# Kernel optimization log

Hardware: AMD Instinct MI355X
Metric: run time of the kernel (lower is better)

## Reference

```python
import jax, jax.numpy as jnp
import numpy as np

N_NODES = 100000
N_EDGES = 625000
D = 128


def setup_inputs() -> dict:
    key = jax.random.key(0)
    ks = jax.random.split(key, 6)
    x = jax.random.normal(ks[0], (N_NODES, D), dtype=jnp.float32)
    src = jax.random.randint(ks[1], (N_EDGES,), 0, N_NODES, dtype=jnp.int32)
    dst = jnp.sort(jax.random.randint(ks[2], (N_EDGES,), 0, N_NODES, dtype=jnp.int32))
    edge_w = jax.random.uniform(ks[3], (N_EDGES,), dtype=jnp.float32)
    # linear layer params (fan-in scaled)
    W = jax.random.normal(ks[4], (D, D), dtype=jnp.float32) / np.sqrt(D)
    b = jnp.zeros((D,), dtype=jnp.float32)
    # highway gate params (glorot-uniform-ish range as in source)
    init_range = np.sqrt(2.0 / (D + D)).astype(np.float32)
    kernel_gate = jax.random.uniform(ks[5], (D, D), dtype=jnp.float32,
                                     minval=-init_range, maxval=init_range)
    bias_gate = jnp.zeros((D,), dtype=jnp.float32)
    return {"x": x, "src": src, "dst": dst, "edge_w": edge_w,
            "W": W, "b": b, "kernel_gate": kernel_gate, "bias_gate": bias_gate}


def reference(x, src, dst, edge_w, W, b, kernel_gate, bias_gate):
    # hidden = Linear(x); dropout is identity in eval mode
    hidden = x @ W.T + b                                  # [N, D]
    # support = spmm(adj, hidden): gather src rows, weight, scatter-add to dst
    msgs = edge_w[:, None] * hidden[src]                  # [E, D]
    support = jax.ops.segment_sum(msgs, dst, num_segments=x.shape[0])
    support = jax.nn.relu(support)                        # act
    # highway gate
    gate = jax.nn.sigmoid(x @ kernel_gate + bias_gate)    # [N, D]
    out = gate * support + (1.0 - gate) * x
    return out
```

## Files before the change

kernel.cpp:

```cpp
#include <hip/hip_runtime.h>

#define DD 128

typedef __attribute__((ext_vector_type(8))) short bf16x8;
typedef __attribute__((ext_vector_type(4))) float f32x4;

__device__ __forceinline__ unsigned int cvt_pk_bf16(float lo, float hi) {
  unsigned int r;
  asm("v_cvt_pk_bf16_f32 %0, %1, %2" : "=v"(r) : "v"(lo), "v"(hi));
  return r;
}
__device__ __forceinline__ float bf_lo(unsigned int v) { return __uint_as_float(v << 16); }
__device__ __forceinline__ float bf_hi(unsigned int v) { return __uint_as_float(v & 0xFFFF0000u); }

__global__ __launch_bounds__(256) void prep_kernel(
    const float* __restrict__ x, const int* __restrict__ dst,
    const float* __restrict__ W, const float* __restrict__ KG,
    unsigned short* __restrict__ xb, unsigned char* __restrict__ xq,
    float* __restrict__ sx, int* __restrict__ row_start,
    unsigned short* __restrict__ B, int N, int E, int ABLK, int BBLK) {
  int blk = blockIdx.x;
  int t = threadIdx.x;
  if (blk < ABLK) {
    int n = blk * 16 + (t >> 4);
    int lr = t & 15;
    if (n < N) {
      const float4* xr = (const float4*)(x + (size_t)n * DD);
      float4 va = xr[lr * 2], vb = xr[lr * 2 + 1];
      float m = fmaxf(fmaxf(fmaxf(fabsf(va.x), fabsf(va.y)), fmaxf(fabsf(va.z), fabsf(va.w))),
                      fmaxf(fmaxf(fabsf(vb.x), fabsf(vb.y)), fmaxf(fabsf(vb.z), fabsf(vb.w))));
#pragma unroll
      for (int d = 1; d < 16; d <<= 1) m = fmaxf(m, __shfl_xor(m, d, 16));
      m = fmaxf(m, 1e-20f);
      float inv = 127.0f / m;
      unsigned int q0 = (unsigned int)(__float2int_rn(va.x * inv) + 128);
      unsigned int q1 = (unsigned int)(__float2int_rn(va.y * inv) + 128);
      unsigned int q2 = (unsigned int)(__float2int_rn(va.z * inv) + 128);
      unsigned int q3 = (unsigned int)(__float2int_rn(va.w * inv) + 128);
      unsigned int q4 = (unsigned int)(__float2int_rn(vb.x * inv) + 128);
      unsigned int q5 = (unsigned int)(__float2int_rn(vb.y * inv) + 128);
      unsigned int q6 = (unsigned int)(__float2int_rn(vb.z * inv) + 128);
      unsigned int q7 = (unsigned int)(__float2int_rn(vb.w * inv) + 128);
      uint2 qp;
      qp.x = q0 | (q1 << 8) | (q2 << 16) | (q3 << 24);
      qp.y = q4 | (q5 << 8) | (q6 << 16) | (q7 << 24);
      ((uint2*)xq)[(size_t)n * 16 + lr] = qp;
      uint4 bp;
      bp.x = cvt_pk_bf16(va.x, va.y);
      bp.y = cvt_pk_bf16(va.z, va.w);
      bp.z = cvt_pk_bf16(vb.x, vb.y);
      bp.w = cvt_pk_bf16(vb.z, vb.w);
      ((uint4*)xb)[(size_t)n * 16 + lr] = bp;
      if (lr == 0) sx[n] = m * (1.0f / 127.0f);
    }
  } else if (blk < ABLK + BBLK) {
    int e = (blk - ABLK) * 256 + t;
    if (e <= E) {
      if (e == 0) {
        int d0 = dst[0];
        for (int n = 0; n <= d0; ++n) row_start[n] = 0;
      } else if (e == E) {
        for (int n = dst[E - 1] + 1; n <= N; ++n) row_start[n] = E;
      } else {
        int d = dst[e], dp = dst[e - 1];
        for (int n = dp + 1; n <= d; ++n) row_start[n] = e;
      }
    }
  } else {
    int e2 = (blk - ABLK - BBLK) * 256 + t;
    if (e2 < 2 * DD * DD) {
      int j = e2 >> 7, k = e2 & 127;
      float v = (j < DD) ? W[j * DD + k] : KG[k * DD + (j - DD)];
      B[e2] = (unsigned short)cvt_pk_bf16(v, v);
    }
  }
}

__global__ __launch_bounds__(256, 8) void scatter_agg(
    const unsigned char* __restrict__ xq, const float* __restrict__ sx,
    const int* __restrict__ src, const float* __restrict__ ew,
    const int* __restrict__ row_start, unsigned short* __restrict__ aggb,
    float* __restrict__ sumw, int N, int E) {
  int t = threadIdx.x;
  int wid = t >> 6, lane = t & 63;
  int g = lane >> 4, lr = lane & 15;
  int n = blockIdx.x * 16 + wid * 4 + g;
  bool valid = (n < N);
  int b = valid ? row_start[n] : 0;
  int cnt = valid ? (row_start[n + 1] - b) : 0;
  const uint2* x8 = (const uint2*)xq;

  float a[8];
#pragma unroll
  for (int k = 0; k < 8; ++k) a[k] = 0.f;
  float wsum = 0.f, wsc = 0.f;
  int clampj = cnt > 0 ? cnt - 1 : 0;

  int i = 0;
  while (__any(i < cnt)) {
#pragma unroll
    for (int u = 0; u < 4; ++u) {
      int ii = i + u;
      int jj = ii < clampj ? ii : clampj;
      int j = b + jj;
      if (j > E - 1) j = E - 1;
      float wt = (ii < cnt) ? ew[j] : 0.f;
      int s = src[j];
      float ws = wt * sx[s];
      uint2 v = x8[(size_t)s * 16 + lr];
      wsum += wt;
      wsc += ws;
      a[0] += ws * (float)(v.x & 0xFF);
      a[1] += ws * (float)((v.x >> 8) & 0xFF);
      a[2] += ws * (float)((v.x >> 16) & 0xFF);
      a[3] += ws * (float)(v.x >> 24);
      a[4] += ws * (float)(v.y & 0xFF);
      a[5] += ws * (float)((v.y >> 8) & 0xFF);
      a[6] += ws * (float)((v.y >> 16) & 0xFF);
      a[7] += ws * (float)(v.y >> 24);
    }
    i += 4;
  }
  float c = 128.0f * wsc;
#pragma unroll
  for (int k = 0; k < 8; ++k) a[k] -= c;

  if (valid) {
    uint4 o;
    o.x = cvt_pk_bf16(a[0], a[1]);
    o.y = cvt_pk_bf16(a[2], a[3]);
    o.z = cvt_pk_bf16(a[4], a[5]);
    o.w = cvt_pk_bf16(a[6], a[7]);
    ((uint4*)aggb)[(size_t)n * 16 + lr] = o;
    if (lr == 0) sumw[n] = wsum;
  }
}

__global__ __launch_bounds__(256, 4) void fused_gemm(
    const unsigned short* __restrict__ xb, const unsigned short* __restrict__ aggb,
    const unsigned short* __restrict__ B, const float* __restrict__ sumw,
    const float* __restrict__ bias, const float* __restrict__ bg,
    float* __restrict__ out, int N) {
  __shared__ char smem[32 * 1024];
  unsigned short* sX = (unsigned short*)smem;
  unsigned short* sA = (unsigned short*)(smem + 16384);
  int t = threadIdx.x;
  int wid = t >> 6, lane = t & 63;
  int lr = lane & 15, lk2 = lane >> 4;
  int jw = wid * 32;
  int M0 = blockIdx.x * 64;

#pragma unroll
  for (int i = 0; i < 4; ++i) {
    int idx = i * 256 + t;
    int r = idx >> 4, c = idx & 15;
    uint4 vx, va;
    if (M0 + r < N) {
      vx = ((const uint4*)(xb + (size_t)(M0 + r) * DD))[c];
      va = ((const uint4*)(aggb + (size_t)(M0 + r) * DD))[c];
    } else {
      vx = make_uint4(0, 0, 0, 0);
      va = make_uint4(0, 0, 0, 0);
    }
    int off = (r * 256 + c * 16) ^ ((r & 7) << 4);
    *(uint4*)((char*)sX + off) = vx;
    *(uint4*)((char*)sA + off) = va;
  }
  __syncthreads();

  f32x4 accS[2][4], accG[2][4];
#pragma unroll
  for (int m = 0; m < 2; ++m)
#pragma unroll
    for (int nr = 0; nr < 4; ++nr) {
      accS[m][nr] = (f32x4){0.f, 0.f, 0.f, 0.f};
      accG[m][nr] = (f32x4){0.f, 0.f, 0.f, 0.f};
    }

#pragma unroll
  for (int kc = 0; kc < 4; ++kc) {
    int kb = (kc * 32 + lk2 * 8) * 2;
    bf16x8 wSk[2], wGk[2];
#pragma unroll
    for (int m = 0; m < 2; ++m) {
      int j = jw + m * 16 + lr;
      wSk[m] = *(const bf16x8*)(B + (size_t)j * DD + kc * 32 + lk2 * 8);
      wGk[m] = *(const bf16x8*)(B + (size_t)(DD + j) * DD + kc * 32 + lk2 * 8);
    }
    bf16x8 af[4], xf[4];
#pragma unroll
    for (int nr = 0; nr < 4; ++nr) {
      int r = nr * 16 + lr;
      int off = (r * 256 + kb) ^ ((r & 7) << 4);
      af[nr] = *(const bf16x8*)((const char*)sA + off);
      xf[nr] = *(const bf16x8*)((const char*)sX + off);
    }
#pragma unroll
    for (int m = 0; m < 2; ++m)
#pragma unroll
      for (int nr = 0; nr < 4; ++nr) {
        accS[m][nr] = __builtin_amdgcn_mfma_f32_16x16x32_bf16(wSk[m], af[nr], accS[m][nr], 0, 0, 0);
        accG[m][nr] = __builtin_amdgcn_mfma_f32_16x16x32_bf16(wGk[m], xf[nr], accG[m][nr], 0, 0, 0);
      }
  }

#pragma unroll
  for (int m = 0; m < 2; ++m) {
    int j0 = jw + m * 16 + lk2 * 4;
    float4 b4 = *(const float4*)&bias[j0];
    float4 bg4 = *(const float4*)&bg[j0];
    float ba[4] = {b4.x, b4.y, b4.z, b4.w};
    float bga[4] = {bg4.x, bg4.y, bg4.z, bg4.w};
#pragma unroll
    for (int nr = 0; nr < 4; ++nr) {
      int node = M0 + nr * 16 + lr;
      if (node < N) {
        float sw = sumw[node];
        int r = nr * 16 + lr;
        uint2 qx = *(const uint2*)((const char*)sX + ((r * 256 + j0 * 2) ^ ((r & 7) << 4)));
        float xr[4] = {bf_lo(qx.x), bf_hi(qx.x), bf_lo(qx.y), bf_hi(qx.y)};
        f32x4 vs = accS[m][nr], vg = accG[m][nr];
        float4 o;
        float* op = &o.x;
#pragma unroll
        for (int reg = 0; reg < 4; ++reg) {
          float s = fmaxf(vs[reg] + sw * ba[reg], 0.f);
          float g = 1.0f / (1.0f + __expf(-(vg[reg] + bga[reg])));
          op[reg] = g * s + (1.0f - g) * xr[reg];
        }
        *(float4*)&out[(size_t)node * DD + j0] = o;
      }
    }
  }
}

extern "C" void kernel_launch(void* const* d_in, const int* in_sizes, int n_in,
                              void* d_out, int out_size, void* d_ws, size_t ws_size,
                              hipStream_t stream) {
  const float* x   = (const float*)d_in[0];
  const int*   src = (const int*)d_in[1];
  const int*   dst = (const int*)d_in[2];
  const float* ew  = (const float*)d_in[3];
  const float* W   = (const float*)d_in[4];
  const float* b   = (const float*)d_in[5];
  const float* KG  = (const float*)d_in[6];
  const float* bg  = (const float*)d_in[7];
  float* out = (float*)d_out;

  int N = in_sizes[0] / DD;
  int E = in_sizes[1];

  unsigned short* xb = (unsigned short*)d_ws;
  unsigned short* aggb = xb + (size_t)N * DD;
  unsigned char* xq = (unsigned char*)(aggb + (size_t)N * DD);
  float* sx = (float*)(xq + (size_t)N * DD);
  float* sumw = sx + N;
  unsigned short* B = (unsigned short*)(sumw + N);
  int* row_start = (int*)(B + 2 * DD * DD);

  int ABLK = (N + 15) / 16;
  int BBLK = (E + 1 + 255) / 256;
  int CBLK = (2 * DD * DD + 255) / 256;
  prep_kernel<<<ABLK + BBLK + CBLK, 256, 0, stream>>>(x, dst, W, KG, xb, xq, sx,
                                                      row_start, B, N, E, ABLK, BBLK);
  scatter_agg<<<(N + 15) / 16, 256, 0, stream>>>(xq, sx, src, ew, row_start, aggb, sumw, N, E);
  fused_gemm<<<(N + 63) / 64, 256, 0, stream>>>(xb, aggb, B, sumw, b, bg, out, N);
}
```

Measured before the change: 80.90 us.

## Convert x to bf16 inside GEMM kernel instead of staging bf16 copy

Removes the bf16 copy of x written by the prep kernel and read back by the fused GEMM. The GEMM now loads fp32 x directly, converts it to bf16 into shared memory, and reads fp32 x again for the highway blend, which also uses exact values. Gate/linear weight fragments are hoisted into registers before the main loop, with launch bounds relaxed to 3 blocks per SM. The cost is reading twice as many bytes for x in the GEMM plus the epilogue re-read, and lower occupancy from higher register use.

```diff
diff --git a/kernel.cpp b/kernel.cpp
--- a/kernel.cpp
+++ b/kernel.cpp
@@ -16,9 +16,9 @@
 __global__ __launch_bounds__(256) void prep_kernel(
     const float* __restrict__ x, const int* __restrict__ dst,
     const float* __restrict__ W, const float* __restrict__ KG,
-    unsigned short* __restrict__ xb, unsigned char* __restrict__ xq,
-    float* __restrict__ sx, int* __restrict__ row_start,
-    unsigned short* __restrict__ B, int N, int E, int ABLK, int BBLK) {
+    unsigned char* __restrict__ xq, float* __restrict__ sx,
+    int* __restrict__ row_start, unsigned short* __restrict__ B,
+    int N, int E, int ABLK, int BBLK) {
   int blk = blockIdx.x;
   int t = threadIdx.x;
   if (blk < ABLK) {
@@ -45,12 +45,6 @@
       qp.x = q0 | (q1 << 8) | (q2 << 16) | (q3 << 24);
       qp.y = q4 | (q5 << 8) | (q6 << 16) | (q7 << 24);
       ((uint2*)xq)[(size_t)n * 16 + lr] = qp;
-      uint4 bp;
-      bp.x = cvt_pk_bf16(va.x, va.y);
-      bp.y = cvt_pk_bf16(va.z, va.w);
-      bp.z = cvt_pk_bf16(vb.x, vb.y);
-      bp.w = cvt_pk_bf16(vb.z, vb.w);
-      ((uint4*)xb)[(size_t)n * 16 + lr] = bp;
       if (lr == 0) sx[n] = m * (1.0f / 127.0f);
     }
   } else if (blk < ABLK + BBLK) {
@@ -136,8 +130,8 @@
   }
 }
 
-__global__ __launch_bounds__(256, 4) void fused_gemm(
-    const unsigned short* __restrict__ xb, const unsigned short* __restrict__ aggb,
+__global__ __launch_bounds__(256, 3) void fused_gemm(
+    const float* __restrict__ x, const unsigned short* __restrict__ aggb,
     const unsigned short* __restrict__ B, const float* __restrict__ sumw,
     const float* __restrict__ bias, const float* __restrict__ bg,
     float* __restrict__ out, int N) {
@@ -150,20 +144,38 @@
   int jw = wid * 32;
   int M0 = blockIdx.x * 64;
 
+  bf16x8 wS[4][2], wG[4][2];
+#pragma unroll
+  for (int kc = 0; kc < 4; ++kc)
+#pragma unroll
+    for (int m = 0; m < 2; ++m) {
+      int j = jw + m * 16 + lr;
+      wS[kc][m] = *(const bf16x8*)(B + (size_t)j * DD + kc * 32 + lk2 * 8);
+      wG[kc][m] = *(const bf16x8*)(B + (size_t)(DD + j) * DD + kc * 32 + lk2 * 8);
+    }
+
+#pragma unroll
+  for (int i = 0; i < 8; ++i) {
+    int f4 = i * 256 + t;
+    int r = f4 >> 5;
+    int kk = (f4 & 31) * 4;
+    float4 v;
+    if (M0 + r < N) v = ((const float4*)x)[(size_t)(M0 + r) * 32 + (f4 & 31)];
+    else            v = make_float4(0.f, 0.f, 0.f, 0.f);
+    unsigned int lo = cvt_pk_bf16(v.x, v.y);
+    unsigned int hi = cvt_pk_bf16(v.z, v.w);
+    int off = (r * 256 + kk * 2) ^ ((r & 7) << 4);
+    uint2 q = {lo, hi};
+    *(uint2*)((char*)sX + off) = q;
+  }
 #pragma unroll
   for (int i = 0; i < 4; ++i) {
     int idx = i * 256 + t;
     int r = idx >> 4, c = idx & 15;
-    uint4 vx, va;
-    if (M0 + r < N) {
-      vx = ((const uint4*)(xb + (size_t)(M0 + r) * DD))[c];
-      va = ((const uint4*)(aggb + (size_t)(M0 + r) * DD))[c];
-    } else {
-      vx = make_uint4(0, 0, 0, 0);
-      va = make_uint4(0, 0, 0, 0);
-    }
+    uint4 va;
+    if (M0 + r < N) va = ((const uint4*)(aggb + (size_t)(M0 + r) * DD))[c];
+    else            va = make_uint4(0, 0, 0, 0);
     int off = (r * 256 + c * 16) ^ ((r & 7) << 4);
-    *(uint4*)((char*)sX + off) = vx;
     *(uint4*)((char*)sA + off) = va;
   }
   __syncthreads();
@@ -180,13 +192,6 @@
 #pragma unroll
   for (int kc = 0; kc < 4; ++kc) {
     int kb = (kc * 32 + lk2 * 8) * 2;
-    bf16x8 wSk[2], wGk[2];
-#pragma unroll
-    for (int m = 0; m < 2; ++m) {
-      int j = jw + m * 16 + lr;
-      wSk[m] = *(const bf16x8*)(B + (size_t)j * DD + kc * 32 + lk2 * 8);
-      wGk[m] = *(const bf16x8*)(B + (size_t)(DD + j) * DD + kc * 32 + lk2 * 8);
-    }
     bf16x8 af[4], xf[4];
 #pragma unroll
     for (int nr = 0; nr < 4; ++nr) {
@@ -199,8 +204,8 @@
     for (int m = 0; m < 2; ++m)
 #pragma unroll
       for (int nr = 0; nr < 4; ++nr) {
-        accS[m][nr] = __builtin_amdgcn_mfma_f32_16x16x32_bf16(wSk[m], af[nr], accS[m][nr], 0, 0, 0);
-        accG[m][nr] = __builtin_amdgcn_mfma_f32_16x16x32_bf16(wGk[m], xf[nr], accG[m][nr], 0, 0, 0);
+        accS[m][nr] = __builtin_amdgcn_mfma_f32_16x16x32_bf16(wS[kc][m], af[nr], accS[m][nr], 0, 0, 0);
+        accG[m][nr] = __builtin_amdgcn_mfma_f32_16x16x32_bf16(wG[kc][m], xf[nr], accG[m][nr], 0, 0, 0);
       }
   }
 
@@ -216,9 +221,8 @@
       int node = M0 + nr * 16 + lr;
       if (node < N) {
         float sw = sumw[node];
-        int r = nr * 16 + lr;
-        uint2 qx = *(const uint2*)((const char*)sX + ((r * 256 + j0 * 2) ^ ((r & 7) << 4)));
-        float xr[4] = {bf_lo(qx.x), bf_hi(qx.x), bf_lo(qx.y), bf_hi(qx.y)};
+        float4 xv = *(const float4*)&x[(size_t)node * DD + j0];
+        float xr[4] = {xv.x, xv.y, xv.z, xv.w};
         f32x4 vs = accS[m][nr], vg = accG[m][nr];
         float4 o;
         float* op = &o.x;
@@ -250,8 +254,7 @@
   int N = in_sizes[0] / DD;
   int E = in_sizes[1];
 
-  unsigned short* xb = (unsigned short*)d_ws;
-  unsigned short* aggb = xb + (size_t)N * DD;
+  unsigned short* aggb = (unsigned short*)d_ws;
   unsigned char* xq = (unsigned char*)(aggb + (size_t)N * DD);
   float* sx = (float*)(xq + (size_t)N * DD);
   float* sumw = sx + N;
@@ -261,8 +264,8 @@
   int ABLK = (N + 15) / 16;
   int BBLK = (E + 1 + 255) / 256;
   int CBLK = (2 * DD * DD + 255) / 256;
-  prep_kernel<<<ABLK + BBLK + CBLK, 256, 0, stream>>>(x, dst, W, KG, xb, xq, sx,
+  prep_kernel<<<ABLK + BBLK + CBLK, 256, 0, stream>>>(x, dst, W, KG, xq, sx,
                                                       row_start, B, N, E, ABLK, BBLK);
   scatter_agg<<<(N + 15) / 16, 256, 0, stream>>>(xq, sx, src, ew, row_start, aggb, sumw, N, E);
-  fused_gemm<<<(N + 63) / 64, 256, 0, stream>>>(xb, aggb, B, sumw, b, bg, out, N);
-}
+  fused_gemm<<<(N + 63) / 64, 256, 0, stream>>>(x, aggb, B, sumw, b, bg, out, N);
+}
```

Result: slower. 92.15 us (+13.9%).
